# Kernel tuning notes

Measured on AMD Instinct MI355X. Metric: run time of the kernel, lower is better.

## Reference

```python
import jax, jax.numpy as jnp
import numpy as np

D = 256
N = 4096


def setup_inputs() -> dict:
    key = jax.random.key(0)
    k0, k1, k2, k3, k4 = jax.random.split(key, 5)
    x0 = jax.random.normal(k0, (N, D), dtype=jnp.float32)
    x1 = jax.random.normal(k1, (N, D), dtype=jnp.float32)
    C_norm = jax.random.normal(k2, (D, D), dtype=jnp.float32)
    # Stacked params of the d Linear(1, d) layers: W[i, j] = weight of layer i
    # mapping scalar input to output unit j; B[i, j] = its bias.
    W = jax.random.normal(k3, (D, D), dtype=jnp.float32) * 0.1
    B = jax.random.normal(k4, (D, D), dtype=jnp.float32) * 0.1
    return {"x0": x0, "x1": x1, "C_norm": C_norm, "W": W, "B": B}


def reference(x0, x1, C_norm, W, B):
    # Original: y[i, j, k] = W[i, j] * x0[k, i] + B[i, j] + C_norm[i, j]
    # then cat x1^T (as a (1, d, n) slab) in front and take max over axis 0.
    # y: (d, d, n)
    y = W[:, :, None] * x0.T[:, None, :] + (B + C_norm)[:, :, None]
    m = jnp.max(y, axis=0)              # (d, n): max over the d source layers
    out = jnp.maximum(m, x1.T)          # include the x1 slab in the max
    return out.T                        # (n, d)
```

## Files before the change

### kernel.cpp

```cpp
#include <hip/hip_runtime.h>


typedef _Float16 h16;
typedef h16 h2  __attribute__((ext_vector_type(2)));
typedef h16 h8v __attribute__((ext_vector_type(8)));
typedef float f32x4 __attribute__((ext_vector_type(4)));

constexpr int Dk = 256;

__global__ __launch_bounds__(256)
void prep(const float* __restrict__ x0, const float* __restrict__ Cn,
          const float* __restrict__ W, const float* __restrict__ Bm,
          h16* __restrict__ x0h, h16* __restrict__ Wh, h16* __restrict__ Ah) {
  const int b = blockIdx.x;
  const int t = threadIdx.x;
  if (b < 512) {
    const int idx = (b * 256 + t) * 8;
    const f32x4 v0 = *reinterpret_cast<const f32x4*>(&x0[idx]);
    const f32x4 v1 = *reinterpret_cast<const f32x4*>(&x0[idx + 4]);
    h8v h;
#pragma unroll
    for (int u = 0; u < 4; ++u) { h[u] = (h16)v0[u]; h[u + 4] = (h16)v1[u]; }
    *reinterpret_cast<h8v*>(&x0h[idx]) = h;
  } else {
    const int idx = ((b - 512) * 256 + t) * 8;
    const f32x4 w0 = *reinterpret_cast<const f32x4*>(&W[idx]);
    const f32x4 w1 = *reinterpret_cast<const f32x4*>(&W[idx + 4]);
    const f32x4 b0 = *reinterpret_cast<const f32x4*>(&Bm[idx]);
    const f32x4 b1 = *reinterpret_cast<const f32x4*>(&Bm[idx + 4]);
    const f32x4 c0 = *reinterpret_cast<const f32x4*>(&Cn[idx]);
    const f32x4 c1 = *reinterpret_cast<const f32x4*>(&Cn[idx + 4]);
    const f32x4 a0 = b0 + c0, a1 = b1 + c1;
    h8v hw, ha;
#pragma unroll
    for (int u = 0; u < 4; ++u) {
      hw[u] = (h16)w0[u]; hw[u + 4] = (h16)w1[u];
      ha[u] = (h16)a0[u]; ha[u + 4] = (h16)a1[u];
    }
    *reinterpret_cast<h8v*>(&Wh[idx]) = hw;
    *reinterpret_cast<h8v*>(&Ah[idx]) = ha;
  }
}

__global__ __launch_bounds__(512, 1)
void mp_main(const h16* __restrict__ x0h, const h16* __restrict__ Wh,
             const h16* __restrict__ Ah, const float* __restrict__ x1,
             float* __restrict__ out) {
  __shared__ h16 Wl[256 * 64];
  __shared__ h16 Al[256 * 64];
  __shared__ h16 Xl[64 * 256];

  const int tid = threadIdx.x;
  const int w   = tid >> 6;
  const int l   = tid & 63;
  const int tk  = l >> 3;
  const int tj  = l & 7;
  const int k0  = (blockIdx.x >> 2) * 64;
  const int j0  = (blockIdx.x & 3) * 64;

#pragma unroll
  for (int c = 0; c < 4; ++c) {
    const int idx = c * 512 + tid;
    const int row = idx >> 3;
    const int col = (idx & 7) * 8;
    *reinterpret_cast<h8v*>(&Wl[row * 64 + col]) =
        *reinterpret_cast<const h8v*>(&Wh[row * Dk + j0 + col]);
    *reinterpret_cast<h8v*>(&Al[row * 64 + col]) =
        *reinterpret_cast<const h8v*>(&Ah[row * Dk + j0 + col]);
  }
#pragma unroll
  for (int c = 0; c < 4; ++c) {
    const int idx = c * 512 + tid;
    const int row = idx >> 5;
    const int col = (idx & 31) * 8;
    const int sw  = col ^ (((row >> 3) & 7) * 8);
    *reinterpret_cast<h8v*>(&Xl[row * 256 + sw]) =
        *reinterpret_cast<const h8v*>(&x0h[(k0 + row) * Dk + col]);
  }
  __syncthreads();

  h2 acc[8][4];
#pragma unroll
  for (int kk = 0; kk < 8; ++kk)
#pragma unroll
    for (int p = 0; p < 4; ++p)
      acc[kk][p] = h2{(h16)(-60000.0f), (h16)(-60000.0f)};

  const int ibase = 32 * w;

#define USTEP(U) {                                                              \
    const h8v wv = *reinterpret_cast<const h8v*>(&Wl[(ic + (U)) * 64 + tj * 8]);\
    const h8v av = *reinterpret_cast<const h8v*>(&Al[(ic + (U)) * 64 + tj * 8]);\
    const h2 wp0 = __builtin_shufflevector(wv, wv, 0, 1);                       \
    const h2 wp1 = __builtin_shufflevector(wv, wv, 2, 3);                       \
    const h2 wp2 = __builtin_shufflevector(wv, wv, 4, 5);                       \
    const h2 wp3 = __builtin_shufflevector(wv, wv, 6, 7);                       \
    const h2 ap0 = __builtin_shufflevector(av, av, 0, 1);                       \
    const h2 ap1 = __builtin_shufflevector(av, av, 2, 3);                       \
    const h2 ap2 = __builtin_shufflevector(av, av, 4, 5);                       \
    const h2 ap3 = __builtin_shufflevector(av, av, 6, 7);                       \
    _Pragma("unroll")                                                           \
    for (int kk = 0; kk < 8; ++kk) {                                            \
      const h2 xb = __builtin_shufflevector(xr[kk], xr[kk], (U), (U));          \
      acc[kk][0] = __builtin_elementwise_max(acc[kk][0], __builtin_elementwise_fma(wp0, xb, ap0)); \
      acc[kk][1] = __builtin_elementwise_max(acc[kk][1], __builtin_elementwise_fma(wp1, xb, ap1)); \
      acc[kk][2] = __builtin_elementwise_max(acc[kk][2], __builtin_elementwise_fma(wp2, xb, ap2)); \
      acc[kk][3] = __builtin_elementwise_max(acc[kk][3], __builtin_elementwise_fma(wp3, xb, ap3)); \
    }                                                                           \
  }

#pragma unroll
  for (int g = 0; g < 4; ++g) {
    const int ic = ibase + g * 8;
    h8v xr[8];
#pragma unroll
    for (int kk = 0; kk < 8; ++kk) {
      const int row = tk * 8 + kk;
      xr[kk] = *reinterpret_cast<const h8v*>(&Xl[row * 256 + (ic ^ (tk * 8))]);
    }
    USTEP(0) USTEP(1) USTEP(2) USTEP(3) USTEP(4) USTEP(5) USTEP(6) USTEP(7)
  }
#undef USTEP
  __syncthreads();

  uint4* mrg = reinterpret_cast<uint4*>(Wl);
  auto wslot = [&](int s) {
#pragma unroll
    for (int kk = 0; kk < 8; ++kk) {
      uint4 u;
      u.x = __builtin_bit_cast(unsigned int, acc[kk][0]);
      u.y = __builtin_bit_cast(unsigned int, acc[kk][1]);
      u.z = __builtin_bit_cast(unsigned int, acc[kk][2]);
      u.w = __builtin_bit_cast(unsigned int, acc[kk][3]);
      mrg[(s * 8 + kk) * 64 + l] = u;
    }
  };
  auto rmerge = [&](int s) {
#pragma unroll
    for (int kk = 0; kk < 8; ++kk) {
      const uint4 u = mrg[(s * 8 + kk) * 64 + l];
      acc[kk][0] = __builtin_elementwise_max(acc[kk][0], __builtin_bit_cast(h2, u.x));
      acc[kk][1] = __builtin_elementwise_max(acc[kk][1], __builtin_bit_cast(h2, u.y));
      acc[kk][2] = __builtin_elementwise_max(acc[kk][2], __builtin_bit_cast(h2, u.z));
      acc[kk][3] = __builtin_elementwise_max(acc[kk][3], __builtin_bit_cast(h2, u.w));
    }
  };

  if (w >= 4) wslot(w - 4);
  __syncthreads();
  if (w < 4) rmerge(w);
  __syncthreads();
  if (w == 2 || w == 3) wslot(w - 2);
  __syncthreads();
  if (w < 2) rmerge(w);
  __syncthreads();
  if (w == 1) wslot(0);
  __syncthreads();
  if (w == 0) { rmerge(0); wslot(0); }
  __syncthreads();

  {
    const uint4 u = mrg[w * 64 + l];
    const h2 p0 = __builtin_bit_cast(h2, u.x);
    const h2 p1 = __builtin_bit_cast(h2, u.y);
    const h2 p2 = __builtin_bit_cast(h2, u.z);
    const h2 p3 = __builtin_bit_cast(h2, u.w);
    const int k = k0 + (l >> 3) * 8 + w;
    const int j = j0 + (l & 7) * 8;
    f32x4 o0 = { (float)p0[0], (float)p0[1], (float)p1[0], (float)p1[1] };
    f32x4 o1 = { (float)p2[0], (float)p2[1], (float)p3[0], (float)p3[1] };
    const f32x4* xg = reinterpret_cast<const f32x4*>(&x1[k * Dk + j]);
    o0 = __builtin_elementwise_max(o0, xg[0]);
    o1 = __builtin_elementwise_max(o1, xg[1]);
    f32x4* og = reinterpret_cast<f32x4*>(&out[k * Dk + j]);
    og[0] = o0;
    og[1] = o1;
  }
}

extern "C" void kernel_launch(void* const* d_in, const int* in_sizes, int n_in,
                              void* d_out, int out_size, void* d_ws, size_t ws_size,
                              hipStream_t stream) {
  const float* x0 = (const float*)d_in[0];
  const float* x1 = (const float*)d_in[1];
  const float* Cn = (const float*)d_in[2];
  const float* W  = (const float*)d_in[3];
  const float* Bm = (const float*)d_in[4];
  float* out = (float*)d_out;

  const int n = in_sizes[0] / Dk;
  h16* x0h = (h16*)d_ws;
  h16* Wh  = (h16*)((char*)d_ws + (size_t)n * Dk * 2);
  h16* Ah  = (h16*)((char*)d_ws + (size_t)n * Dk * 2 + Dk * Dk * 2);

  hipLaunchKernelGGL(prep, dim3(512 + 32), dim3(256), 0, stream,
                     x0, Cn, W, Bm, x0h, Wh, Ah);
  hipLaunchKernelGGL(mp_main, dim3((n / 64) * 4), dim3(512), 0, stream,
                     x0h, Wh, Ah, x1, out);
}
```

Baseline: 23.96 us.

## Transpose x0 in prep and stream W/A rows through registers instead of LDS

The prep kernel now writes x0 transposed to fp16 ([i][k] layout) through an LDS tile. The main kernel keeps only a 32 KB X tile in shared memory and loads W and A rows straight from global memory into registers, double-buffering the second half of the rows while the first half is computed. Each wave now covers a different split of the i dimension. The goal is to cut LDS footprint from 96 KB to 32 KB so that two blocks can reside per CU (launch_bounds 512,2), and to reduce LDS traffic. The costs are heavier register pressure from holding 32 h8v vectors, plus global reads of W/A issued from every block. N is also hardcoded to 4096.

Result: slower. 24.97 us (+4.2%).

```diff
diff --git a/kernel.cpp b/kernel.cpp
--- a/kernel.cpp
+++ b/kernel.cpp
@@ -7,23 +7,39 @@
 typedef float f32x4 __attribute__((ext_vector_type(4)));
 
 constexpr int Dk = 256;
+constexpr int NK = 4096;
 
 __global__ __launch_bounds__(256)
 void prep(const float* __restrict__ x0, const float* __restrict__ Cn,
           const float* __restrict__ W, const float* __restrict__ Bm,
-          h16* __restrict__ x0h, h16* __restrict__ Wh, h16* __restrict__ Ah) {
+          h16* __restrict__ x0T, h16* __restrict__ Wh, h16* __restrict__ Ah) {
   const int b = blockIdx.x;
   const int t = threadIdx.x;
-  if (b < 512) {
-    const int idx = (b * 256 + t) * 8;
-    const f32x4 v0 = *reinterpret_cast<const f32x4*>(&x0[idx]);
-    const f32x4 v1 = *reinterpret_cast<const f32x4*>(&x0[idx + 4]);
-    h8v h;
-#pragma unroll
-    for (int u = 0; u < 4; ++u) { h[u] = (h16)v0[u]; h[u + 4] = (h16)v1[u]; }
-    *reinterpret_cast<h8v*>(&x0h[idx]) = h;
+  if (b < 256) {
+    __shared__ float tl[64][65];
+    const int kt = b >> 2;
+    const int it = b & 3;
+#pragma unroll
+    for (int q = 0; q < 4; ++q) {
+      const int idx = q * 256 + t;
+      const int row = idx >> 4;
+      const int c4  = (idx & 15) * 4;
+      *reinterpret_cast<f32x4*>(&tl[row][c4]) =
+          *reinterpret_cast<const f32x4*>(&x0[(kt * 64 + row) * Dk + it * 64 + c4]);
+    }
+    __syncthreads();
+#pragma unroll
+    for (int q = 0; q < 2; ++q) {
+      const int c = q * 256 + t;
+      const int i  = c >> 3;
+      const int k8 = (c & 7) * 8;
+      h8v h;
+#pragma unroll
+      for (int u = 0; u < 8; ++u) h[u] = (h16)tl[k8 + u][i];
+      *reinterpret_cast<h8v*>(&x0T[(size_t)(it * 64 + i) * NK + kt * 64 + k8]) = h;
+    }
   } else {
-    const int idx = ((b - 512) * 256 + t) * 8;
+    const int idx = ((b - 256) * 256 + t) * 8;
     const f32x4 w0 = *reinterpret_cast<const f32x4*>(&W[idx]);
     const f32x4 w1 = *reinterpret_cast<const f32x4*>(&W[idx + 4]);
     const f32x4 b0 = *reinterpret_cast<const f32x4*>(&Bm[idx]);
@@ -42,13 +58,11 @@
   }
 }
 
-__global__ __launch_bounds__(512, 1)
-void mp_main(const h16* __restrict__ x0h, const h16* __restrict__ Wh,
+__global__ __launch_bounds__(512, 2)
+void mp_main(const h16* __restrict__ x0T, const h16* __restrict__ Wh,
              const h16* __restrict__ Ah, const float* __restrict__ x1,
              float* __restrict__ out) {
-  __shared__ h16 Wl[256 * 64];
-  __shared__ h16 Al[256 * 64];
-  __shared__ h16 Xl[64 * 256];
+  __shared__ h16 Xl[256 * 64];
 
   const int tid = threadIdx.x;
   const int w   = tid >> 6;
@@ -58,24 +72,21 @@
   const int k0  = (blockIdx.x >> 2) * 64;
   const int j0  = (blockIdx.x & 3) * 64;
 
-#pragma unroll
-  for (int c = 0; c < 4; ++c) {
-    const int idx = c * 512 + tid;
-    const int row = idx >> 3;
-    const int col = (idx & 7) * 8;
-    *reinterpret_cast<h8v*>(&Wl[row * 64 + col]) =
-        *reinterpret_cast<const h8v*>(&Wh[row * Dk + j0 + col]);
-    *reinterpret_cast<h8v*>(&Al[row * 64 + col]) =
-        *reinterpret_cast<const h8v*>(&Ah[row * Dk + j0 + col]);
-  }
-#pragma unroll
-  for (int c = 0; c < 4; ++c) {
-    const int idx = c * 512 + tid;
-    const int row = idx >> 5;
-    const int col = (idx & 31) * 8;
-    const int sw  = col ^ (((row >> 3) & 7) * 8);
-    *reinterpret_cast<h8v*>(&Xl[row * 256 + sw]) =
-        *reinterpret_cast<const h8v*>(&x0h[(k0 + row) * Dk + col]);
+  h8v wr[16], ar[16];
+#pragma unroll
+  for (int r = 0; r < 16; ++r) {
+    const int i = w * 16 + r;
+    wr[r] = *reinterpret_cast<const h8v*>(&Wh[i * Dk + j0 + tj * 8]);
+    ar[r] = *reinterpret_cast<const h8v*>(&Ah[i * Dk + j0 + tj * 8]);
+  }
+
+#pragma unroll
+  for (int p = 0; p < 4; ++p) {
+    const int c  = p * 512 + tid;
+    const int ir = c >> 3;
+    const int k8 = (c & 7) * 8;
+    const h8v v = *reinterpret_cast<const h8v*>(&x0T[(size_t)ir * NK + k0 + k8]);
+    *reinterpret_cast<h8v*>(&Xl[ir * 64 + k8]) = v;
   }
   __syncthreads();
 
@@ -86,44 +97,45 @@
     for (int p = 0; p < 4; ++p)
       acc[kk][p] = h2{(h16)(-60000.0f), (h16)(-60000.0f)};
 
-  const int ibase = 32 * w;
-
-#define USTEP(U) {                                                              \
-    const h8v wv = *reinterpret_cast<const h8v*>(&Wl[(ic + (U)) * 64 + tj * 8]);\
-    const h8v av = *reinterpret_cast<const h8v*>(&Al[(ic + (U)) * 64 + tj * 8]);\
-    const h2 wp0 = __builtin_shufflevector(wv, wv, 0, 1);                       \
-    const h2 wp1 = __builtin_shufflevector(wv, wv, 2, 3);                       \
-    const h2 wp2 = __builtin_shufflevector(wv, wv, 4, 5);                       \
-    const h2 wp3 = __builtin_shufflevector(wv, wv, 6, 7);                       \
-    const h2 ap0 = __builtin_shufflevector(av, av, 0, 1);                       \
-    const h2 ap1 = __builtin_shufflevector(av, av, 2, 3);                       \
-    const h2 ap2 = __builtin_shufflevector(av, av, 4, 5);                       \
-    const h2 ap3 = __builtin_shufflevector(av, av, 6, 7);                       \
-    _Pragma("unroll")                                                           \
-    for (int kk = 0; kk < 8; ++kk) {                                            \
-      const h2 xb = __builtin_shufflevector(xr[kk], xr[kk], (U), (U));          \
-      acc[kk][0] = __builtin_elementwise_max(acc[kk][0], __builtin_elementwise_fma(wp0, xb, ap0)); \
-      acc[kk][1] = __builtin_elementwise_max(acc[kk][1], __builtin_elementwise_fma(wp1, xb, ap1)); \
-      acc[kk][2] = __builtin_elementwise_max(acc[kk][2], __builtin_elementwise_fma(wp2, xb, ap2)); \
-      acc[kk][3] = __builtin_elementwise_max(acc[kk][3], __builtin_elementwise_fma(wp3, xb, ap3)); \
-    }                                                                           \
-  }
-
-#pragma unroll
-  for (int g = 0; g < 4; ++g) {
-    const int ic = ibase + g * 8;
-    h8v xr[8];
-#pragma unroll
-    for (int kk = 0; kk < 8; ++kk) {
-      const int row = tk * 8 + kk;
-      xr[kk] = *reinterpret_cast<const h8v*>(&Xl[row * 256 + (ic ^ (tk * 8))]);
-    }
-    USTEP(0) USTEP(1) USTEP(2) USTEP(3) USTEP(4) USTEP(5) USTEP(6) USTEP(7)
-  }
-#undef USTEP
-  __syncthreads();
-
-  uint4* mrg = reinterpret_cast<uint4*>(Wl);
+#define KSTEP(K) {                                                              \
+    const h2 xb = __builtin_shufflevector(xrv, xrv, (K), (K));                  \
+    acc[K][0] = __builtin_elementwise_max(acc[K][0], __builtin_elementwise_fma(wp0, xb, ap0)); \
+    acc[K][1] = __builtin_elementwise_max(acc[K][1], __builtin_elementwise_fma(wp1, xb, ap1)); \
+    acc[K][2] = __builtin_elementwise_max(acc[K][2], __builtin_elementwise_fma(wp2, xb, ap2)); \
+    acc[K][3] = __builtin_elementwise_max(acc[K][3], __builtin_elementwise_fma(wp3, xb, ap3)); \
+  }
+
+#define RSTEP(WV, AV) {                                                         \
+    const h2 wp0 = __builtin_shufflevector(WV, WV, 0, 1);                       \
+    const h2 wp1 = __builtin_shufflevector(WV, WV, 2, 3);                       \
+    const h2 wp2 = __builtin_shufflevector(WV, WV, 4, 5);                       \
+    const h2 wp3 = __builtin_shufflevector(WV, WV, 6, 7);                       \
+    const h2 ap0 = __builtin_shufflevector(AV, AV, 0, 1);                       \
+    const h2 ap1 = __builtin_shufflevector(AV, AV, 2, 3);                       \
+    const h2 ap2 = __builtin_shufflevector(AV, AV, 4, 5);                       \
+    const h2 ap3 = __builtin_shufflevector(AV, AV, 6, 7);                       \
+    KSTEP(0) KSTEP(1) KSTEP(2) KSTEP(3) KSTEP(4) KSTEP(5) KSTEP(6) KSTEP(7)    \
+  }
+
+#pragma unroll
+  for (int r = 0; r < 16; ++r) {
+    const h8v xrv = *reinterpret_cast<const h8v*>(&Xl[(w * 16 + r) * 64 + tk * 8]);
+    RSTEP(wr[r], ar[r])
+    const int i1 = 128 + w * 16 + r;
+    wr[r] = *reinterpret_cast<const h8v*>(&Wh[i1 * Dk + j0 + tj * 8]);
+    ar[r] = *reinterpret_cast<const h8v*>(&Ah[i1 * Dk + j0 + tj * 8]);
+  }
+#pragma unroll
+  for (int r = 0; r < 16; ++r) {
+    const h8v xrv = *reinterpret_cast<const h8v*>(&Xl[(128 + w * 16 + r) * 64 + tk * 8]);
+    RSTEP(wr[r], ar[r])
+  }
+#undef RSTEP
+#undef KSTEP
+
+  __syncthreads();
+
+  uint4* mrg = reinterpret_cast<uint4*>(Xl);
   auto wslot = [&](int s) {
 #pragma unroll
     for (int kk = 0; kk < 8; ++kk) {
@@ -188,13 +200,12 @@
   const float* Bm = (const float*)d_in[4];
   float* out = (float*)d_out;
 
-  const int n = in_sizes[0] / Dk;
-  h16* x0h = (h16*)d_ws;
-  h16* Wh  = (h16*)((char*)d_ws + (size_t)n * Dk * 2);
-  h16* Ah  = (h16*)((char*)d_ws + (size_t)n * Dk * 2 + Dk * Dk * 2);
-
-  hipLaunchKernelGGL(prep, dim3(512 + 32), dim3(256), 0, stream,
-                     x0, Cn, W, Bm, x0h, Wh, Ah);
-  hipLaunchKernelGGL(mp_main, dim3((n / 64) * 4), dim3(512), 0, stream,
-                     x0h, Wh, Ah, x1, out);
+  h16* x0T = (h16*)d_ws;
+  h16* Wh  = (h16*)((char*)d_ws + (size_t)NK * Dk * 2);
+  h16* Ah  = (h16*)((char*)d_ws + (size_t)NK * Dk * 2 + Dk * Dk * 2);
+
+  hipLaunchKernelGGL(prep, dim3(256 + 32), dim3(256), 0, stream,
+                     x0, Cn, W, Bm, x0T, Wh, Ah);
+  hipLaunchKernelGGL(mp_main, dim3((NK / 64) * 4), dim3(512), 0, stream,
+                     x0T, Wh, Ah, x1, out);
 }
```

## Retile main kernel to 64x32 output tiles with 16-way i split and 4 blocks/CU

Applied to the files above, without the earlier changes.

The main kernel moves from 64x64 output tiles (256 blocks) to 64x32 tiles (512 blocks). The i-reduction is split across 16 half-wave groups of 32 threads instead of 8 waves, and W/A fragments are held in registers while looping over x rows. Shared memory shrinks to 64 KB and launch bounds now request 4 blocks per CU, aiming for higher occupancy and more blocks in flight on the device. The trade-off is a deeper cross-group max-merge tree with more barriers, an XOR-swizzled merge buffer, and the problem size hardcoded as N=4096.

Result: slower. 26.45 us (+10.4%).

```diff
diff --git a/kernel.cpp b/kernel.cpp
--- a/kernel.cpp
+++ b/kernel.cpp
@@ -7,13 +7,13 @@
 typedef float f32x4 __attribute__((ext_vector_type(4)));
 
 constexpr int Dk = 256;
+constexpr int NK = 4096;
 
 __global__ __launch_bounds__(256)
 void prep(const float* __restrict__ x0, const float* __restrict__ Cn,
           const float* __restrict__ W, const float* __restrict__ Bm,
           h16* __restrict__ x0h, h16* __restrict__ Wh, h16* __restrict__ Ah) {
-  const int b = blockIdx.x;
-  const int t = threadIdx.x;
+  const int b = blockIdx.x, t = threadIdx.x;
   if (b < 512) {
     const int idx = (b * 256 + t) * 8;
     const f32x4 v0 = *reinterpret_cast<const f32x4*>(&x0[idx]);
@@ -42,40 +42,38 @@
   }
 }
 
-__global__ __launch_bounds__(512, 1)
+__global__ __launch_bounds__(512, 4)
 void mp_main(const h16* __restrict__ x0h, const h16* __restrict__ Wh,
              const h16* __restrict__ Ah, const float* __restrict__ x1,
              float* __restrict__ out) {
-  __shared__ h16 Wl[256 * 64];
-  __shared__ h16 Al[256 * 64];
-  __shared__ h16 Xl[64 * 256];
+  __shared__ __align__(16) h16 smem[32768];
+  h16* Xl = smem;
+  h16* Wl = smem + 16384;
+  h16* Al = smem + 24576;
 
   const int tid = threadIdx.x;
-  const int w   = tid >> 6;
-  const int l   = tid & 63;
-  const int tk  = l >> 3;
-  const int tj  = l & 7;
-  const int k0  = (blockIdx.x >> 2) * 64;
-  const int j0  = (blockIdx.x & 3) * 64;
+  const int s   = tid >> 5;
+  const int t5  = tid & 31;
+  const int tk  = t5 >> 2;
+  const int tj  = t5 & 3;
+  const int k0  = (blockIdx.x >> 3) * 64;
+  const int j0  = (blockIdx.x & 7) * 32;
 
 #pragma unroll
   for (int c = 0; c < 4; ++c) {
     const int idx = c * 512 + tid;
-    const int row = idx >> 3;
-    const int col = (idx & 7) * 8;
-    *reinterpret_cast<h8v*>(&Wl[row * 64 + col]) =
-        *reinterpret_cast<const h8v*>(&Wh[row * Dk + j0 + col]);
-    *reinterpret_cast<h8v*>(&Al[row * 64 + col]) =
-        *reinterpret_cast<const h8v*>(&Ah[row * Dk + j0 + col]);
+    const int row = idx >> 5, ch = (idx & 31) * 8;
+    *reinterpret_cast<h8v*>(&Xl[row * 256 + ch]) =
+        *reinterpret_cast<const h8v*>(&x0h[(k0 + row) * Dk + ch]);
   }
 #pragma unroll
-  for (int c = 0; c < 4; ++c) {
+  for (int c = 0; c < 2; ++c) {
     const int idx = c * 512 + tid;
-    const int row = idx >> 5;
-    const int col = (idx & 31) * 8;
-    const int sw  = col ^ (((row >> 3) & 7) * 8);
-    *reinterpret_cast<h8v*>(&Xl[row * 256 + sw]) =
-        *reinterpret_cast<const h8v*>(&x0h[(k0 + row) * Dk + col]);
+    const int row = idx >> 2, jc = (idx & 3) * 8;
+    *reinterpret_cast<h8v*>(&Wl[row * 32 + jc]) =
+        *reinterpret_cast<const h8v*>(&Wh[row * Dk + j0 + jc]);
+    *reinterpret_cast<h8v*>(&Al[row * 32 + jc]) =
+        *reinterpret_cast<const h8v*>(&Ah[row * Dk + j0 + jc]);
   }
   __syncthreads();
 
@@ -86,95 +84,93 @@
     for (int p = 0; p < 4; ++p)
       acc[kk][p] = h2{(h16)(-60000.0f), (h16)(-60000.0f)};
 
-  const int ibase = 32 * w;
-
-#define USTEP(U) {                                                              \
-    const h8v wv = *reinterpret_cast<const h8v*>(&Wl[(ic + (U)) * 64 + tj * 8]);\
-    const h8v av = *reinterpret_cast<const h8v*>(&Al[(ic + (U)) * 64 + tj * 8]);\
-    const h2 wp0 = __builtin_shufflevector(wv, wv, 0, 1);                       \
-    const h2 wp1 = __builtin_shufflevector(wv, wv, 2, 3);                       \
-    const h2 wp2 = __builtin_shufflevector(wv, wv, 4, 5);                       \
-    const h2 wp3 = __builtin_shufflevector(wv, wv, 6, 7);                       \
-    const h2 ap0 = __builtin_shufflevector(av, av, 0, 1);                       \
-    const h2 ap1 = __builtin_shufflevector(av, av, 2, 3);                       \
-    const h2 ap2 = __builtin_shufflevector(av, av, 4, 5);                       \
-    const h2 ap3 = __builtin_shufflevector(av, av, 6, 7);                       \
-    _Pragma("unroll")                                                           \
-    for (int kk = 0; kk < 8; ++kk) {                                            \
-      const h2 xb = __builtin_shufflevector(xr[kk], xr[kk], (U), (U));          \
-      acc[kk][0] = __builtin_elementwise_max(acc[kk][0], __builtin_elementwise_fma(wp0, xb, ap0)); \
-      acc[kk][1] = __builtin_elementwise_max(acc[kk][1], __builtin_elementwise_fma(wp1, xb, ap1)); \
-      acc[kk][2] = __builtin_elementwise_max(acc[kk][2], __builtin_elementwise_fma(wp2, xb, ap2)); \
-      acc[kk][3] = __builtin_elementwise_max(acc[kk][3], __builtin_elementwise_fma(wp3, xb, ap3)); \
-    }                                                                           \
+#define USTEP(U) {                                                               \
+    const h2 xb = __builtin_shufflevector(xv, xv, (U), (U));                     \
+    const h2 w0 = __builtin_shufflevector(wv[U], wv[U], 0, 1);                   \
+    const h2 w1 = __builtin_shufflevector(wv[U], wv[U], 2, 3);                   \
+    const h2 w2 = __builtin_shufflevector(wv[U], wv[U], 4, 5);                   \
+    const h2 w3 = __builtin_shufflevector(wv[U], wv[U], 6, 7);                   \
+    const h2 a0 = __builtin_shufflevector(av[U], av[U], 0, 1);                   \
+    const h2 a1 = __builtin_shufflevector(av[U], av[U], 2, 3);                   \
+    const h2 a2 = __builtin_shufflevector(av[U], av[U], 4, 5);                   \
+    const h2 a3 = __builtin_shufflevector(av[U], av[U], 6, 7);                   \
+    acc[kk][0] = __builtin_elementwise_max(acc[kk][0], __builtin_elementwise_fma(w0, xb, a0)); \
+    acc[kk][1] = __builtin_elementwise_max(acc[kk][1], __builtin_elementwise_fma(w1, xb, a1)); \
+    acc[kk][2] = __builtin_elementwise_max(acc[kk][2], __builtin_elementwise_fma(w2, xb, a2)); \
+    acc[kk][3] = __builtin_elementwise_max(acc[kk][3], __builtin_elementwise_fma(w3, xb, a3)); \
   }
 
 #pragma unroll
-  for (int g = 0; g < 4; ++g) {
-    const int ic = ibase + g * 8;
-    h8v xr[8];
+  for (int cc = 0; cc < 2; ++cc) {
+    const int i0 = s * 16 + cc * 8;
+    h8v wv[8], av[8];
+#pragma unroll
+    for (int u = 0; u < 8; ++u) {
+      wv[u] = *reinterpret_cast<const h8v*>(&Wl[(i0 + u) * 32 + tj * 8]);
+      av[u] = *reinterpret_cast<const h8v*>(&Al[(i0 + u) * 32 + tj * 8]);
+    }
 #pragma unroll
     for (int kk = 0; kk < 8; ++kk) {
-      const int row = tk * 8 + kk;
-      xr[kk] = *reinterpret_cast<const h8v*>(&Xl[row * 256 + (ic ^ (tk * 8))]);
+      const h8v xv = *reinterpret_cast<const h8v*>(&Xl[(tk * 8 + kk) * 256 + i0]);
+      USTEP(0) USTEP(1) USTEP(2) USTEP(3) USTEP(4) USTEP(5) USTEP(6) USTEP(7)
     }
-    USTEP(0) USTEP(1) USTEP(2) USTEP(3) USTEP(4) USTEP(5) USTEP(6) USTEP(7)
   }
 #undef USTEP
+
   __syncthreads();
 
-  uint4* mrg = reinterpret_cast<uint4*>(Wl);
-  auto wslot = [&](int s) {
+  uint4* mrg = reinterpret_cast<uint4*>(smem);
+  auto wslot = [&](int slot) {
 #pragma unroll
-    for (int kk = 0; kk < 8; ++kk) {
+    for (int c = 0; c < 8; ++c) {
       uint4 u;
-      u.x = __builtin_bit_cast(unsigned int, acc[kk][0]);
-      u.y = __builtin_bit_cast(unsigned int, acc[kk][1]);
-      u.z = __builtin_bit_cast(unsigned int, acc[kk][2]);
-      u.w = __builtin_bit_cast(unsigned int, acc[kk][3]);
-      mrg[(s * 8 + kk) * 64 + l] = u;
+      u.x = __builtin_bit_cast(unsigned int, acc[c][0]);
+      u.y = __builtin_bit_cast(unsigned int, acc[c][1]);
+      u.z = __builtin_bit_cast(unsigned int, acc[c][2]);
+      u.w = __builtin_bit_cast(unsigned int, acc[c][3]);
+      mrg[(slot * 32 + t5) * 8 + (c ^ (t5 & 7))] = u;
     }
   };
-  auto rmerge = [&](int s) {
+  auto rmerge = [&](int slot) {
 #pragma unroll
-    for (int kk = 0; kk < 8; ++kk) {
-      const uint4 u = mrg[(s * 8 + kk) * 64 + l];
-      acc[kk][0] = __builtin_elementwise_max(acc[kk][0], __builtin_bit_cast(h2, u.x));
-      acc[kk][1] = __builtin_elementwise_max(acc[kk][1], __builtin_bit_cast(h2, u.y));
-      acc[kk][2] = __builtin_elementwise_max(acc[kk][2], __builtin_bit_cast(h2, u.z));
-      acc[kk][3] = __builtin_elementwise_max(acc[kk][3], __builtin_bit_cast(h2, u.w));
+    for (int c = 0; c < 8; ++c) {
+      const uint4 u = mrg[(slot * 32 + t5) * 8 + (c ^ (t5 & 7))];
+      acc[c][0] = __builtin_elementwise_max(acc[c][0], __builtin_bit_cast(h2, u.x));
+      acc[c][1] = __builtin_elementwise_max(acc[c][1], __builtin_bit_cast(h2, u.y));
+      acc[c][2] = __builtin_elementwise_max(acc[c][2], __builtin_bit_cast(h2, u.z));
+      acc[c][3] = __builtin_elementwise_max(acc[c][3], __builtin_bit_cast(h2, u.w));
     }
   };
 
-  if (w >= 4) wslot(w - 4);
+  if (s >= 8) wslot(s - 8);
   __syncthreads();
-  if (w < 4) rmerge(w);
+  if (s < 8) rmerge(s);
   __syncthreads();
-  if (w == 2 || w == 3) wslot(w - 2);
+  if (s >= 4 && s < 8) wslot(s - 4);
   __syncthreads();
-  if (w < 2) rmerge(w);
+  if (s < 4) rmerge(s);
   __syncthreads();
-  if (w == 1) wslot(0);
+  if (s == 2 || s == 3) wslot(s - 2);
   __syncthreads();
-  if (w == 0) { rmerge(0); wslot(0); }
+  if (s < 2) rmerge(s);
+  __syncthreads();
+  if (s == 1) wslot(0);
+  __syncthreads();
+  if (s == 0) { rmerge(0); wslot(0); }
   __syncthreads();
 
   {
-    const uint4 u = mrg[w * 64 + l];
-    const h2 p0 = __builtin_bit_cast(h2, u.x);
-    const h2 p1 = __builtin_bit_cast(h2, u.y);
-    const h2 p2 = __builtin_bit_cast(h2, u.z);
-    const h2 p3 = __builtin_bit_cast(h2, u.w);
-    const int k = k0 + (l >> 3) * 8 + w;
-    const int j = j0 + (l & 7) * 8;
-    f32x4 o0 = { (float)p0[0], (float)p0[1], (float)p1[0], (float)p1[1] };
-    f32x4 o1 = { (float)p2[0], (float)p2[1], (float)p3[0], (float)p3[1] };
-    const f32x4* xg = reinterpret_cast<const f32x4*>(&x1[k * Dk + j]);
-    o0 = __builtin_elementwise_max(o0, xg[0]);
-    o1 = __builtin_elementwise_max(o1, xg[1]);
-    f32x4* og = reinterpret_cast<f32x4*>(&out[k * Dk + j]);
-    og[0] = o0;
-    og[1] = o1;
+    const int kr  = tid >> 3;
+    const int jq  = tid & 7;
+    const int ot5 = (kr >> 3) * 4 + (jq >> 1);
+    const int oc  = kr & 7;
+    const uint4 u = mrg[ot5 * 8 + (oc ^ (ot5 & 7))];
+    const h2 pa = __builtin_bit_cast(h2, (jq & 1) ? u.z : u.x);
+    const h2 pb = __builtin_bit_cast(h2, (jq & 1) ? u.w : u.y);
+    const int k = k0 + kr, j = j0 + jq * 4;
+    f32x4 o = { (float)pa[0], (float)pa[1], (float)pb[0], (float)pb[1] };
+    o = __builtin_elementwise_max(o, *reinterpret_cast<const f32x4*>(&x1[k * Dk + j]));
+    *reinterpret_cast<f32x4*>(&out[k * Dk + j]) = o;
   }
 }
 
@@ -188,13 +184,12 @@
   const float* Bm = (const float*)d_in[4];
   float* out = (float*)d_out;
 
-  const int n = in_sizes[0] / Dk;
   h16* x0h = (h16*)d_ws;
-  h16* Wh  = (h16*)((char*)d_ws + (size_t)n * Dk * 2);
-  h16* Ah  = (h16*)((char*)d_ws + (size_t)n * Dk * 2 + Dk * Dk * 2);
+  h16* Wh  = (h16*)((char*)d_ws + (size_t)NK * Dk * 2);
+  h16* Ah  = (h16*)((char*)d_ws + (size_t)NK * Dk * 2 + Dk * Dk * 2);
 
   hipLaunchKernelGGL(prep, dim3(512 + 32), dim3(256), 0, stream,
                      x0, Cn, W, Bm, x0h, Wh, Ah);
-  hipLaunchKernelGGL(mp_main, dim3((n / 64) * 4), dim3(512), 0, stream,
+  hipLaunchKernelGGL(mp_main, dim3((NK / 64) * 8), dim3(512), 0, stream,
                      x0h, Wh, Ah, x1, out);
 }
```
